# Kernel tuning notes

Hardware: AMD Instinct MI355X
Metric: run time of the kernel (lower is better)

## Reference

```python
import jax, jax.numpy as jnp
import numpy as np

L, D, H, DH, FF, V, B, T, WD, BAND = 4, 512, 8, 64, 2048, 32000, 2, 1024, 32, 128
SCALE = 1.0 / float(np.sqrt(DH))

# per-head causal masks: even heads full causal, odd heads banded causal (0 <= i-j < BAND)
_diff = np.arange(T)[:, None] - np.arange(T)[None, :]
_full = _diff >= 0
_band = _full & (_diff < BAND)
MASKS = jnp.asarray(np.where((np.arange(H) % 2 == 0)[:, None, None], _full, _band))  # (H,T,T) bool
# ALiBi slopes for H=8 (power of 2): start=ratio=2^(-2^(-(log2(8)-3)))=0.5 -> 0.5^(1..8)
_slopes = 0.5 ** np.arange(1, H + 1)
ALIBI = jnp.asarray((-_slopes[:, None, None] * _diff).astype(np.float32))  # (H,T,T)


def _ln(x, g, b):
    m = x.mean(-1, keepdims=True)
    v = ((x - m) ** 2).mean(-1, keepdims=True)
    return (x - m) / jnp.sqrt(v + 1e-5) * g + b


def setup_inputs() -> dict:
    key = jax.random.key(0)
    ks = jax.random.split(key, 16)
    s = 0.02
    n = lambda k, shape: jax.random.normal(k, shape, jnp.float32) * s
    return dict(
        idx=jax.random.randint(ks[0], (B, T), 0, V),
        wte=n(ks[1], (V, D)), wpe=n(ks[2], (T, D)),
        ln1_g=jnp.ones((L, D)), ln1_b=jnp.zeros((L, D)),
        attn_w=n(ks[3], (L, 3 * D, D)), attn_b=jnp.zeros((L, 3 * D)),
        proj_w=n(ks[4], (L, D, D)), proj_b=jnp.zeros((L, D)),
        dape_gw=n(ks[5], (L, WD, 2 * H)), dape_gb=jnp.zeros((L, WD)),
        dape_vw=n(ks[6], (L, WD, 2 * H)), dape_vb=jnp.zeros((L, WD)),
        dape_ow=n(ks[7], (L, H, WD)), dape_ob=jnp.zeros((L, H)),
        ln2_g=jnp.ones((L, D)), ln2_b=jnp.zeros((L, D)),
        gate_w=n(ks[8], (L, FF, D)), gate_b=jnp.zeros((L, FF)),
        val_w=n(ks[9], (L, FF, D)), val_b=jnp.zeros((L, FF)),
        mlp_w=n(ks[10], (L, D, FF)), mlp_b=jnp.zeros((L, D)),
        lnf_g=jnp.ones((D,)), lnf_b=jnp.zeros((D,)),
        lm_w=n(ks[11], (V, D)),
    )


def reference(idx, wte, wpe, ln1_g, ln1_b, attn_w, attn_b, proj_w, proj_b,
              dape_gw, dape_gb, dape_vw, dape_vb, dape_ow, dape_ob,
              ln2_g, ln2_b, gate_w, gate_b, val_w, val_b, mlp_w, mlp_b,
              lnf_g, lnf_b, lm_w):
    x = wte[idx] + wpe[jnp.arange(T)][None]  # (B,T,D)
    for l in range(L):
        h = _ln(x, ln1_g[l], ln1_b[l])
        qkv = h @ attn_w[l].T + attn_b[l]
        q, k, v = jnp.split(qkv, 3, axis=-1)
        q = q.reshape(B, T, H, DH).transpose(0, 2, 1, 3)
        k = k.reshape(B, T, H, DH).transpose(0, 2, 1, 3)
        v = v.reshape(B, T, H, DH).transpose(0, 2, 1, 3)
        att = jnp.einsum('bhqd,bhkd->bhqk', q, k) * SCALE  # (B,H,T,T)
        # DAPE: concat(att, zero base bias) along head dim, pointwise SWIGLU MLP 2H->WD->H
        cat = jnp.concatenate([att, jnp.zeros_like(att)], axis=1).transpose(0, 2, 3, 1)  # (B,T,T,2H)
        hid = jax.nn.silu(cat @ dape_gw[l].T + dape_gb[l]) * (cat @ dape_vw[l].T + dape_vb[l])
        lb = hid @ dape_ow[l].T + dape_ob[l]  # (B,T,T,H)
        att = att + lb.transpose(0, 3, 1, 2) + ALIBI[None]
        att = jnp.where(MASKS[None], att, -jnp.inf)
        att = jax.nn.softmax(att, axis=-1)
        y = jnp.einsum('bhqk,bhkd->bhqd', att, v).transpose(0, 2, 1, 3).reshape(B, T, D)
        x = x + y @ proj_w[l].T + proj_b[l]
        h2 = _ln(x, ln2_g[l], ln2_b[l])
        ff = jax.nn.silu(h2 @ gate_w[l].T + gate_b[l]) * (h2 @ val_w[l].T + val_b[l])
        x = x + ff @ mlp_w[l].T + mlp_b[l]
    x = _ln(x, lnf_g, lnf_b)
    return x @ lm_w.T  # (B,T,V)
```

## Files before the change

kernel.cpp:

```cpp
#include <hip/hip_runtime.h>
#include <hip/hip_bf16.h>
#include <math.h>

constexpr int L = 4, D = 512, H = 8, DH = 64, FF = 2048, V = 32000, B = 2, T = 1024, WD = 32, BAND = 128;
constexpr float SCALE = 0.125f;

typedef __hip_bfloat16 bf16;
typedef __attribute__((ext_vector_type(8))) short short8;
typedef __attribute__((ext_vector_type(4))) float floatx4;

#define MFMA16(a, b, c) __builtin_amdgcn_mfma_f32_16x16x32_bf16(a, b, c, 0, 0, 0)

__device__ inline void gl_lds16(const void* g, void* l) {
    __builtin_amdgcn_global_load_lds((const __attribute__((address_space(1))) unsigned int*)g,
                                     (__attribute__((address_space(3))) unsigned int*)l, 16, 0, 0);
}

__global__ __launch_bounds__(256) void embed_k(const int* __restrict__ idx,
                                               const float* __restrict__ wte,
                                               const float* __restrict__ wpe,
                                               float* __restrict__ x) {
    int row = blockIdx.x;
    int t = row % T;
    int token = idx[row];
    const float* we = wte + (size_t)token * D;
    const float* pe = wpe + (size_t)t * D;
    float* xo = x + (size_t)row * D;
    for (int d = threadIdx.x; d < D; d += 256) xo[d] = we[d] + pe[d];
}

__global__ __launch_bounds__(256) void f2b_k(const float* __restrict__ in,
                                             bf16* __restrict__ out, int n4) {
    int i = blockIdx.x * 256 + threadIdx.x;
    if (i >= n4) return;
    float4 v = *(const float4*)&in[(size_t)i * 4];
    bf16 o[4] = {__float2bfloat16(v.x), __float2bfloat16(v.y),
                 __float2bfloat16(v.z), __float2bfloat16(v.w)};
    *(ulong1*)&out[(size_t)i * 4] = *(ulong1*)o;
}

__global__ __launch_bounds__(256) void ln_bf16_k(const float* __restrict__ x,
                                                 const float* __restrict__ g,
                                                 const float* __restrict__ b,
                                                 bf16* __restrict__ o) {
    int row = blockIdx.x;
    const float* xr = x + (size_t)row * D;
    int d0 = threadIdx.x, d1 = threadIdx.x + 256;
    float v0 = xr[d0], v1 = xr[d1];
    float s = v0 + v1, ss = v0 * v0 + v1 * v1;
    for (int off = 32; off > 0; off >>= 1) {
        s  += __shfl_down(s, off);
        ss += __shfl_down(ss, off);
    }
    __shared__ float red[2][4];
    int wid = threadIdx.x >> 6;
    if ((threadIdx.x & 63) == 0) { red[0][wid] = s; red[1][wid] = ss; }
    __syncthreads();
    s  = red[0][0] + red[0][1] + red[0][2] + red[0][3];
    ss = red[1][0] + red[1][1] + red[1][2] + red[1][3];
    float mean = s * (1.0f / D);
    float var  = ss * (1.0f / D) - mean * mean;
    float rstd = rsqrtf(var + 1e-5f);
    bf16* orow = o + (size_t)row * D;
    orow[d0] = __float2bfloat16((v0 - mean) * rstd * g[d0] + b[d0]);
    orow[d1] = __float2bfloat16((v1 - mean) * rstd * g[d1] + b[d1]);
}

template <int EPI>
__global__ __launch_bounds__(256) void mgemm_k(const bf16* __restrict__ A,
                                               const bf16* __restrict__ W,
                                               const float* __restrict__ bias,
                                               const float* res,
                                               float* C, int M, int N, int K) {
    __shared__ __align__(16) bf16 As[128 * 32];
    __shared__ __align__(16) bf16 Bs[128 * 32];
    int tid = threadIdx.x;
    int wave = tid >> 6, lane = tid & 63;
    int quad = lane >> 4, l16 = lane & 15;
    int m0 = blockIdx.y * 128, n0 = blockIdx.x * 128;
    int wm = wave >> 1, wn = wave & 1;
    floatx4 acc[4][4] = {};

    int idx0 = tid, idx1 = tid + 256;
    const bf16* Ag0 = A + (size_t)(m0 + (idx0 >> 2)) * K + (idx0 & 3) * 8;
    const bf16* Ag1 = A + (size_t)(m0 + (idx1 >> 2)) * K + (idx1 & 3) * 8;
    const bf16* Wg0 = W + (size_t)(n0 + (idx0 >> 2)) * K + (idx0 & 3) * 8;
    const bf16* Wg1 = W + (size_t)(n0 + (idx1 >> 2)) * K + (idx1 & 3) * 8;
    bf16* lA0 = As + (size_t)(wave * 64) * 8;
    bf16* lA1 = As + (size_t)(256 + wave * 64) * 8;
    bf16* lB0 = Bs + (size_t)(wave * 64) * 8;
    bf16* lB1 = Bs + (size_t)(256 + wave * 64) * 8;

    for (int k0 = 0; k0 < K; k0 += 32) {
        __syncthreads();
        gl_lds16(Ag0 + k0, lA0);
        gl_lds16(Ag1 + k0, lA1);
        gl_lds16(Wg0 + k0, lB0);
        gl_lds16(Wg1 + k0, lB1);
        __syncthreads();
        short8 a[4], b[4];
#pragma unroll
        for (int mi = 0; mi < 4; mi++)
            a[mi] = *(const short8*)&As[(wm * 64 + mi * 16 + l16) * 32 + quad * 8];
#pragma unroll
        for (int ni = 0; ni < 4; ni++)
            b[ni] = *(const short8*)&Bs[(wn * 64 + ni * 16 + l16) * 32 + quad * 8];
#pragma unroll
        for (int mi = 0; mi < 4; mi++)
#pragma unroll
            for (int ni = 0; ni < 4; ni++)
                acc[mi][ni] = MFMA16(a[mi], b[ni], acc[mi][ni]);
    }

    int row_base = m0 + wm * 64 + quad * 4;
    int col_base = n0 + wn * 64 + l16;
#pragma unroll
    for (int mi = 0; mi < 4; mi++) {
#pragma unroll
        for (int r = 0; r < 4; r++) {
            int m = row_base + mi * 16 + r;
#pragma unroll
            for (int ni = 0; ni < 4; ni++) {
                int n = col_base + ni * 16;
                float v = acc[mi][ni][r];
                if (EPI == 0 || EPI == 1 || EPI == 3) v += bias[n];
                if (EPI == 1) v += res[(size_t)m * N + n];
                if (EPI == 3) {
                    ((bf16*)C)[(size_t)m * N + n] = __float2bfloat16(v);
                } else {
                    C[(size_t)m * N + n] = v;
                }
            }
        }
    }
}

__global__ __launch_bounds__(256) void swiglu_k(const float* __restrict__ g,
                                                const float* __restrict__ v,
                                                bf16* __restrict__ out, int n4) {
    int i = blockIdx.x * 256 + threadIdx.x;
    if (i >= n4) return;
    float4 gv = *(const float4*)&g[(size_t)i * 4];
    float4 vv = *(const float4*)&v[(size_t)i * 4];
    float r0 = gv.x / (1.0f + __expf(-gv.x)) * vv.x;
    float r1 = gv.y / (1.0f + __expf(-gv.y)) * vv.y;
    float r2 = gv.z / (1.0f + __expf(-gv.z)) * vv.z;
    float r3 = gv.w / (1.0f + __expf(-gv.w)) * vv.w;
    bf16 o[4] = {__float2bfloat16(r0), __float2bfloat16(r1),
                 __float2bfloat16(r2), __float2bfloat16(r3)};
    *(ulong1*)&out[(size_t)i * 4] = *(ulong1*)o;
}

__global__ __launch_bounds__(256) void vt_k(const bf16* __restrict__ qkvb,
                                            bf16* __restrict__ vT) {
    int bh = blockIdx.y, b = bh >> 3, h = bh & 7;
    int t0 = blockIdx.x * 64;
    __shared__ bf16 Ls[64][72];
    int tid = threadIdx.x;
#pragma unroll
    for (int it = 0; it < 2; it++) {
        int c = it * 256 + tid;
        int r = c >> 3, s = c & 7;
        *(short8*)&Ls[r][s * 8] =
            *(const short8*)&qkvb[((size_t)(b * T + t0 + r)) * (3 * D) + 2 * D + h * DH + s * 8];
    }
    __syncthreads();
    int d = tid & 63;
    int tg = tid >> 6;
    for (int k = tg; k < 8; k += 4) {
        union { unsigned short u[8]; short8 v; } tmp;
#pragma unroll
        for (int e = 0; e < 8; e++) tmp.u[e] = *(const unsigned short*)&Ls[k * 8 + e][d];
        *(short8*)&vT[((size_t)bh * DH + d) * T + t0 + k * 8] = tmp.v;
    }
}

__global__ __launch_bounds__(256) void qk_mfma_k(const bf16* __restrict__ qkvb,
                                                 float* __restrict__ att) {
    int bh = blockIdx.z; int b = bh >> 3, h = bh & 7;
    int i0 = blockIdx.y * 64, j0 = blockIdx.x * 64;
    if (j0 > i0 + 63) return;
    __shared__ __align__(16) bf16 Qs[64 * 64];
    __shared__ __align__(16) bf16 Ks[64 * 64];
    int tid = threadIdx.x;
    int wave = tid >> 6, lane = tid & 63;
    int l16 = lane & 15, quad = lane >> 4;
    int wi = wave >> 1, wj = wave & 1;

    const bf16* Qbase = qkvb + ((size_t)(b * T + i0)) * (3 * D) + h * DH;
    const bf16* Kbase = qkvb + ((size_t)(b * T + j0)) * (3 * D) + D + h * DH;
#pragma unroll
    for (int it = 0; it < 2; it++) {
        int cbase = it * 256 + wave * 64;
        int c = cbase + lane;
        int r = c >> 3, s = c & 7, gs = s ^ (r & 7);
        gl_lds16(Qbase + (size_t)r * (3 * D) + gs * 8, Qs + (size_t)cbase * 8);
        gl_lds16(Kbase + (size_t)r * (3 * D) + gs * 8, Ks + (size_t)cbase * 8);
    }
    __syncthreads();

    floatx4 acc[2][2] = {};
#pragma unroll
    for (int ks = 0; ks < 2; ks++) {
        short8 a[2], bb[2];
#pragma unroll
        for (int mi = 0; mi < 2; mi++) {
            int row = wi * 32 + mi * 16 + l16;
            a[mi] = *(const short8*)&Qs[row * 64 + (((ks * 4 + quad) ^ (row & 7)) * 8)];
        }
#pragma unroll
        for (int ni = 0; ni < 2; ni++) {
            int row = wj * 32 + ni * 16 + l16;
            bb[ni] = *(const short8*)&Ks[row * 64 + (((ks * 4 + quad) ^ (row & 7)) * 8)];
        }
#pragma unroll
        for (int mi = 0; mi < 2; mi++)
#pragma unroll
            for (int ni = 0; ni < 2; ni++)
                acc[mi][ni] = MFMA16(a[mi], bb[ni], acc[mi][ni]);
    }

    size_t obase = ((size_t)bh * T + (i0 + wi * 32)) * T + (j0 + wj * 32);
#pragma unroll
    for (int mi = 0; mi < 2; mi++)
#pragma unroll
        for (int r = 0; r < 4; r++)
#pragma unroll
            for (int ni = 0; ni < 2; ni++)
                att[obase + (size_t)(mi * 16 + quad * 4 + r) * T + ni * 16 + l16] =
                    acc[mi][ni][r] * SCALE;
}

__global__ __launch_bounds__(256) void dape_sm_k(const float* __restrict__ att,
                                                 bf16* __restrict__ P,
                                                 const float* __restrict__ gw,
                                                 const float* __restrict__ gb,
                                                 const float* __restrict__ vw,
                                                 const float* __restrict__ vb,
                                                 const float* __restrict__ ow,
                                                 const float* __restrict__ ob) {
    int bi = blockIdx.x;
    int b = bi >> 10;
    int i = (T - 1) - (bi & (T - 1));
    int tid = threadIdx.x;
    int wave = tid >> 6, lane = tid & 63;

    __shared__ float4 sgw[WD][2], svw[WD][2], sow[WD][2];
    __shared__ float sgb[WD], svb[WD], sob[H];
    __shared__ float redm[4][8], reds[4][8];
    if (tid < WD) {
        sgw[tid][0] = *(const float4*)&gw[tid * 2 * H];
        sgw[tid][1] = *(const float4*)&gw[tid * 2 * H + 4];
        svw[tid][0] = *(const float4*)&vw[tid * 2 * H];
        svw[tid][1] = *(const float4*)&vw[tid * 2 * H + 4];
        sgb[tid] = gb[tid]; svb[tid] = vb[tid];
        float o0[4], o1[4];
#pragma unroll
        for (int hh = 0; hh < 4; hh++) o0[hh] = ow[hh * WD + tid];
#pragma unroll
        for (int hh = 0; hh < 4; hh++) o1[hh] = ow[(hh + 4) * WD + tid];
        sow[tid][0] = *(float4*)o0;
        sow[tid][1] = *(float4*)o1;
    }
    if (tid < H) sob[tid] = ob[tid];
    __syncthreads();

    const float slopes[8] = {0.5f, 0.25f, 0.125f, 0.0625f,
                             0.03125f, 0.015625f, 0.0078125f, 0.00390625f};
    size_t abase = (size_t)b * H * T * T + (size_t)i * T;

    float sv[4][8];
    int jv[4];
#pragma unroll
    for (int c = 0; c < 4; c++) {
        int j = tid + c * 256;
        jv[c] = j;
        if (j <= i) {
#pragma unroll
            for (int hh = 0; hh < 8; hh++)
                sv[c][hh] = att[abase + (size_t)hh * T * T + j];
        }
    }

    float lb[4][8];
#pragma unroll
    for (int c = 0; c < 4; c++)
#pragma unroll
        for (int hh = 0; hh < 8; hh++) lb[c][hh] = sob[hh];
    for (int w = 0; w < WD; w++) {
        float4 g0 = sgw[w][0], g1 = sgw[w][1];
        float4 v0 = svw[w][0], v1 = svw[w][1];
        float4 o0 = sow[w][0], o1 = sow[w][1];
        float gbb = sgb[w], vbb = svb[w];
#pragma unroll
        for (int c = 0; c < 4; c++) {
            if (jv[c] <= i) {
                float g = gbb + sv[c][0] * g0.x + sv[c][1] * g0.y + sv[c][2] * g0.z + sv[c][3] * g0.w
                              + sv[c][4] * g1.x + sv[c][5] * g1.y + sv[c][6] * g1.z + sv[c][7] * g1.w;
                float v = vbb + sv[c][0] * v0.x + sv[c][1] * v0.y + sv[c][2] * v0.z + sv[c][3] * v0.w
                              + sv[c][4] * v1.x + sv[c][5] * v1.y + sv[c][6] * v1.z + sv[c][7] * v1.w;
                float hid = g / (1.0f + __expf(-g)) * v;
                lb[c][0] += hid * o0.x; lb[c][1] += hid * o0.y;
                lb[c][2] += hid * o0.z; lb[c][3] += hid * o0.w;
                lb[c][4] += hid * o1.x; lb[c][5] += hid * o1.y;
                lb[c][6] += hid * o1.z; lb[c][7] += hid * o1.w;
            }
        }
    }

    float mx[8];
#pragma unroll
    for (int hh = 0; hh < 8; hh++) mx[hh] = -1e30f;
#pragma unroll
    for (int c = 0; c < 4; c++) {
        if (jv[c] <= i) {
            float diff = (float)(i - jv[c]);
#pragma unroll
            for (int hh = 0; hh < 8; hh++) {
                float val = sv[c][hh] + lb[c][hh] - slopes[hh] * diff;
                if ((hh & 1) && (jv[c] < i - (BAND - 1))) val = -1e30f;
                sv[c][hh] = val;
                mx[hh] = fmaxf(mx[hh], val);
            }
        }
    }
    for (int off = 32; off > 0; off >>= 1)
#pragma unroll
        for (int hh = 0; hh < 8; hh++) mx[hh] = fmaxf(mx[hh], __shfl_down(mx[hh], off));
    if (lane == 0)
#pragma unroll
        for (int hh = 0; hh < 8; hh++) redm[wave][hh] = mx[hh];
    __syncthreads();
#pragma unroll
    for (int hh = 0; hh < 8; hh++)
        mx[hh] = fmaxf(fmaxf(redm[0][hh], redm[1][hh]), fmaxf(redm[2][hh], redm[3][hh]));

    float sm[8];
#pragma unroll
    for (int hh = 0; hh < 8; hh++) sm[hh] = 0.f;
#pragma unroll
    for (int c = 0; c < 4; c++) {
        if (jv[c] <= i) {
#pragma unroll
            for (int hh = 0; hh < 8; hh++) {
                float p = __expf(sv[c][hh] - mx[hh]);
                sv[c][hh] = p;
                sm[hh] += p;
            }
        }
    }
    for (int off = 32; off > 0; off >>= 1)
#pragma unroll
        for (int hh = 0; hh < 8; hh++) sm[hh] += __shfl_down(sm[hh], off);
    if (lane == 0)
#pragma unroll
        for (int hh = 0; hh < 8; hh++) reds[wave][hh] = sm[hh];
    __syncthreads();
    float inv[8];
#pragma unroll
    for (int hh = 0; hh < 8; hh++)
        inv[hh] = 1.0f / (reds[0][hh] + reds[1][hh] + reds[2][hh] + reds[3][hh]);

    size_t pbase = (size_t)b * H * T * T + (size_t)i * T;
#pragma unroll
    for (int c = 0; c < 4; c++) {
        if (jv[c] <= i) {
#pragma unroll
            for (int hh = 0; hh < 8; hh++)
                P[pbase + (size_t)hh * T * T + jv[c]] = __float2bfloat16(sv[c][hh] * inv[hh]);
        }
    }
    int ia = i & ~63;
    int zhi = ia + 63;
    for (int j = i + 1 + tid; j <= zhi; j += 256)
#pragma unroll
        for (int hh = 0; hh < 8; hh++)
            P[pbase + (size_t)hh * T * T + j] = __float2bfloat16(0.f);
    int js = (ia - (BAND - 1) > 0 ? ia - (BAND - 1) : 0) & ~31;
    for (int j = js + tid; j <= i - BAND; j += 256)
#pragma unroll
        for (int hh = 1; hh < 8; hh += 2)
            P[pbase + (size_t)hh * T * T + j] = __float2bfloat16(0.f);
}

__global__ __launch_bounds__(256) void av_mfma_k(const bf16* __restrict__ P,
                                                 const bf16* __restrict__ vT,
                                                 bf16* __restrict__ y) {
    int bh = blockIdx.y; int b = bh >> 3, h = bh & 7;
    int ia = blockIdx.x * 64;
    __shared__ __align__(16) bf16 Ps[64 * 32];
    __shared__ __align__(16) bf16 Vs[64 * 32];
    int tid = threadIdx.x, wave = tid >> 6, lane = tid & 63;
    int l16 = lane & 15, quad = lane >> 4;
    int wi = wave >> 1, wn = wave & 1;
    floatx4 acc[2][2] = {};

    int j_end = ia + 63;
    int j_start = (h & 1) ? ((ia - (BAND - 1) > 0 ? ia - (BAND - 1) : 0) & ~31) : 0;
    const bf16* Pbase = P + ((size_t)bh * T + ia) * T;
    const bf16* Vbase = vT + (size_t)bh * DH * T;
    int r = tid >> 2, s = tid & 3, gs = s ^ ((r >> 1) & 3);
    bf16* lP = Ps + (size_t)(wave * 64) * 8;
    bf16* lV = Vs + (size_t)(wave * 64) * 8;

    for (int j0 = j_start; j0 <= j_end; j0 += 32) {
        __syncthreads();
        gl_lds16(Pbase + (size_t)r * T + j0 + gs * 8, lP);
        gl_lds16(Vbase + (size_t)r * T + j0 + gs * 8, lV);
        __syncthreads();
        short8 a[2], bb[2];
#pragma unroll
        for (int mi = 0; mi < 2; mi++) {
            int row = wi * 32 + mi * 16 + l16;
            a[mi] = *(const short8*)&Ps[row * 32 + ((quad ^ ((row >> 1) & 3)) * 8)];
        }
#pragma unroll
        for (int ni = 0; ni < 2; ni++) {
            int row = wn * 32 + ni * 16 + l16;
            bb[ni] = *(const short8*)&Vs[row * 32 + ((quad ^ ((row >> 1) & 3)) * 8)];
        }
#pragma unroll
        for (int mi = 0; mi < 2; mi++)
#pragma unroll
            for (int ni = 0; ni < 2; ni++)
                acc[mi][ni] = MFMA16(a[mi], bb[ni], acc[mi][ni]);
    }

#pragma unroll
    for (int mi = 0; mi < 2; mi++)
#pragma unroll
        for (int rr = 0; rr < 4; rr++) {
            int i = ia + wi * 32 + mi * 16 + quad * 4 + rr;
#pragma unroll
            for (int ni = 0; ni < 2; ni++) {
                int d = wn * 32 + ni * 16 + l16;
                y[((size_t)(b * T + i)) * D + h * DH + d] = __float2bfloat16(acc[mi][ni][rr]);
            }
        }
}

extern "C" void kernel_launch(void* const* d_in, const int* in_sizes, int n_in,
                              void* d_out, int out_size, void* d_ws, size_t ws_size,
                              hipStream_t stream) {
    const int*   idx     = (const int*)d_in[0];
    const float* wte     = (const float*)d_in[1];
    const float* wpe     = (const float*)d_in[2];
    const float* ln1_g   = (const float*)d_in[3];
    const float* ln1_b   = (const float*)d_in[4];
    const float* attn_w  = (const float*)d_in[5];
    const float* attn_b  = (const float*)d_in[6];
    const float* proj_w  = (const float*)d_in[7];
    const float* proj_b  = (const float*)d_in[8];
    const float* dape_gw = (const float*)d_in[9];
    const float* dape_gb = (const float*)d_in[10];
    const float* dape_vw = (const float*)d_in[11];
    const float* dape_vb = (const float*)d_in[12];
    const float* dape_ow = (const float*)d_in[13];
    const float* dape_ob = (const float*)d_in[14];
    const float* ln2_g   = (const float*)d_in[15];
    const float* ln2_b   = (const float*)d_in[16];
    const float* gate_w  = (const float*)d_in[17];
    const float* gate_b  = (const float*)d_in[18];
    const float* val_w   = (const float*)d_in[19];
    const float* val_b   = (const float*)d_in[20];
    const float* mlp_w   = (const float*)d_in[21];
    const float* mlp_b   = (const float*)d_in[22];
    const float* lnf_g   = (const float*)d_in[23];
    const float* lnf_b   = (const float*)d_in[24];
    const float* lm_w    = (const float*)d_in[25];
    float* out = (float*)d_out;

    float* ws   = (float*)d_ws;
    float* x    = ws;
    float* att  = x + (size_t)B * T * D;
    float* gbuf = att;
    float* vbuf = att + (size_t)B * T * FF;
    bf16*  hb   = (bf16*)(att + (size_t)B * H * T * T);
    bf16*  yb   = hb   + (size_t)B * T * D;
    bf16*  ffb  = yb   + (size_t)B * T * D;
    bf16*  qkvb = ffb  + (size_t)B * T * FF;
    bf16*  vTb  = qkvb + (size_t)B * T * 3 * D;
    bf16*  Pb   = vTb  + (size_t)B * H * DH * T;
    bf16*  wq   = Pb   + (size_t)B * H * T * T;
    bf16*  wp   = wq   + (size_t)L * 3 * D * D;
    bf16*  wg   = wp   + (size_t)L * D * D;
    bf16*  wv   = wg   + (size_t)L * FF * D;
    bf16*  wm   = wv   + (size_t)L * FF * D;
    bf16*  wl   = wm   + (size_t)L * D * FF;

    auto conv = [&](const float* src, bf16* dst, size_t n) {
        int n4 = (int)(n / 4);
        f2b_k<<<(n4 + 255) / 256, 256, 0, stream>>>(src, dst, n4);
    };
    conv(attn_w, wq, (size_t)L * 3 * D * D);
    conv(proj_w, wp, (size_t)L * D * D);
    conv(gate_w, wg, (size_t)L * FF * D);
    conv(val_w,  wv, (size_t)L * FF * D);
    conv(mlp_w,  wm, (size_t)L * D * FF);
    conv(lm_w,   wl, (size_t)V * D);

    embed_k<<<B * T, 256, 0, stream>>>(idx, wte, wpe, x);

    const int M = B * T;
    for (int l = 0; l < L; l++) {
        ln_bf16_k<<<M, 256, 0, stream>>>(x, ln1_g + l * D, ln1_b + l * D, hb);
        mgemm_k<3><<<dim3(3 * D / 128, M / 128), 256, 0, stream>>>(
            hb, wq + (size_t)l * 3 * D * D, attn_b + l * 3 * D, nullptr, (float*)qkvb, M, 3 * D, D);
        vt_k<<<dim3(T / 64, B * H), 256, 0, stream>>>(qkvb, vTb);
        qk_mfma_k<<<dim3(T / 64, T / 64, B * H), 256, 0, stream>>>(qkvb, att);
        dape_sm_k<<<B * T, 256, 0, stream>>>(att, Pb,
            dape_gw + l * WD * 2 * H, dape_gb + l * WD,
            dape_vw + l * WD * 2 * H, dape_vb + l * WD,
            dape_ow + l * H * WD, dape_ob + l * H);
        av_mfma_k<<<dim3(T / 64, B * H), 256, 0, stream>>>(Pb, vTb, yb);
        mgemm_k<1><<<dim3(D / 128, M / 128), 256, 0, stream>>>(
            yb, wp + (size_t)l * D * D, proj_b + l * D, x, x, M, D, D);
        ln_bf16_k<<<M, 256, 0, stream>>>(x, ln2_g + l * D, ln2_b + l * D, hb);
        mgemm_k<0><<<dim3(FF / 128, M / 128), 256, 0, stream>>>(
            hb, wg + (size_t)l * FF * D, gate_b + l * FF, nullptr, gbuf, M, FF, D);
        mgemm_k<0><<<dim3(FF / 128, M / 128), 256, 0, stream>>>(
            hb, wv + (size_t)l * FF * D, val_b + l * FF, nullptr, vbuf, M, FF, D);
        {
            int n4 = B * T * FF / 4;
            swiglu_k<<<(n4 + 255) / 256, 256, 0, stream>>>(gbuf, vbuf, ffb, n4);
        }
        mgemm_k<1><<<dim3(D / 128, M / 128), 256, 0, stream>>>(
            ffb, wm + (size_t)l * D * FF, mlp_b + l * D, x, x, M, D, FF);
    }

    ln_bf16_k<<<M, 256, 0, stream>>>(x, lnf_g, lnf_b, hb);
    mgemm_k<2><<<dim3(V / 128, M / 128), 256, 0, stream>>>(
        hb, wl, nullptr, nullptr, out, M, V, D);
}
```

Measured before the change: 1.531 ms.

## Fuse gate/value GEMMs with SwiGLU epilogue and shrink GEMM tiles for small-N

Adds a dual-weight GEMM kernel that computes the gate and value projections together from one shared A tile and applies SiLU-gating in the epilogue, writing bf16 directly. This removes two fp32 intermediate buffers, their round-trip through memory, and the separate swiglu launch. The GEMM kernel is also templated on tile size, and the QKV, proj and MLP-down GEMMs now use 128x64 tiles so more blocks are launched across the CUs. Smaller tiles lower per-block data reuse.

```diff
diff --git a/kernel.cpp b/kernel.cpp
--- a/kernel.cpp
+++ b/kernel.cpp
@@ -66,61 +66,71 @@
     orow[d1] = __float2bfloat16((v1 - mean) * rstd * g[d1] + b[d1]);
 }
 
-template <int EPI>
+template <int BM, int BN, int EPI>
 __global__ __launch_bounds__(256) void mgemm_k(const bf16* __restrict__ A,
                                                const bf16* __restrict__ W,
                                                const float* __restrict__ bias,
                                                const float* res,
                                                float* C, int M, int N, int K) {
-    __shared__ __align__(16) bf16 As[128 * 32];
-    __shared__ __align__(16) bf16 Bs[128 * 32];
+    constexpr int WM = BM / 2, WN = BN / 2;
+    constexpr int FM = WM / 16, FN = WN / 16;
+    constexpr int CA = BM / 64, CB = BN / 64;
+    __shared__ __align__(16) bf16 As[BM * 32];
+    __shared__ __align__(16) bf16 Bs[BN * 32];
     int tid = threadIdx.x;
     int wave = tid >> 6, lane = tid & 63;
     int quad = lane >> 4, l16 = lane & 15;
-    int m0 = blockIdx.y * 128, n0 = blockIdx.x * 128;
+    int m0 = blockIdx.y * BM, n0 = blockIdx.x * BN;
     int wm = wave >> 1, wn = wave & 1;
-    floatx4 acc[4][4] = {};
-
-    int idx0 = tid, idx1 = tid + 256;
-    const bf16* Ag0 = A + (size_t)(m0 + (idx0 >> 2)) * K + (idx0 & 3) * 8;
-    const bf16* Ag1 = A + (size_t)(m0 + (idx1 >> 2)) * K + (idx1 & 3) * 8;
-    const bf16* Wg0 = W + (size_t)(n0 + (idx0 >> 2)) * K + (idx0 & 3) * 8;
-    const bf16* Wg1 = W + (size_t)(n0 + (idx1 >> 2)) * K + (idx1 & 3) * 8;
-    bf16* lA0 = As + (size_t)(wave * 64) * 8;
-    bf16* lA1 = As + (size_t)(256 + wave * 64) * 8;
-    bf16* lB0 = Bs + (size_t)(wave * 64) * 8;
-    bf16* lB1 = Bs + (size_t)(256 + wave * 64) * 8;
+    floatx4 acc[FM][FN] = {};
+
+    const bf16* Ag[CA];
+    const bf16* Wg[CB];
+    bf16* lA[CA];
+    bf16* lB[CB];
+#pragma unroll
+    for (int c = 0; c < CA; c++) {
+        int idx = c * 256 + tid;
+        Ag[c] = A + (size_t)(m0 + (idx >> 2)) * K + (idx & 3) * 8;
+        lA[c] = As + (size_t)(c * 256 + wave * 64) * 8;
+    }
+#pragma unroll
+    for (int c = 0; c < CB; c++) {
+        int idx = c * 256 + tid;
+        Wg[c] = W + (size_t)(n0 + (idx >> 2)) * K + (idx & 3) * 8;
+        lB[c] = Bs + (size_t)(c * 256 + wave * 64) * 8;
+    }
 
     for (int k0 = 0; k0 < K; k0 += 32) {
         __syncthreads();
-        gl_lds16(Ag0 + k0, lA0);
-        gl_lds16(Ag1 + k0, lA1);
-        gl_lds16(Wg0 + k0, lB0);
-        gl_lds16(Wg1 + k0, lB1);
+#pragma unroll
+        for (int c = 0; c < CA; c++) gl_lds16(Ag[c] + k0, lA[c]);
+#pragma unroll
+        for (int c = 0; c < CB; c++) gl_lds16(Wg[c] + k0, lB[c]);
         __syncthreads();
-        short8 a[4], b[4];
-#pragma unroll
-        for (int mi = 0; mi < 4; mi++)
-            a[mi] = *(const short8*)&As[(wm * 64 + mi * 16 + l16) * 32 + quad * 8];
-#pragma unroll
-        for (int ni = 0; ni < 4; ni++)
-            b[ni] = *(const short8*)&Bs[(wn * 64 + ni * 16 + l16) * 32 + quad * 8];
-#pragma unroll
-        for (int mi = 0; mi < 4; mi++)
-#pragma unroll
-            for (int ni = 0; ni < 4; ni++)
+        short8 a[FM], b[FN];
+#pragma unroll
+        for (int mi = 0; mi < FM; mi++)
+            a[mi] = *(const short8*)&As[(wm * WM + mi * 16 + l16) * 32 + quad * 8];
+#pragma unroll
+        for (int ni = 0; ni < FN; ni++)
+            b[ni] = *(const short8*)&Bs[(wn * WN + ni * 16 + l16) * 32 + quad * 8];
+#pragma unroll
+        for (int mi = 0; mi < FM; mi++)
+#pragma unroll
+            for (int ni = 0; ni < FN; ni++)
                 acc[mi][ni] = MFMA16(a[mi], b[ni], acc[mi][ni]);
     }
 
-    int row_base = m0 + wm * 64 + quad * 4;
-    int col_base = n0 + wn * 64 + l16;
-#pragma unroll
-    for (int mi = 0; mi < 4; mi++) {
+    int row_base = m0 + wm * WM + quad * 4;
+    int col_base = n0 + wn * WN + l16;
+#pragma unroll
+    for (int mi = 0; mi < FM; mi++) {
 #pragma unroll
         for (int r = 0; r < 4; r++) {
             int m = row_base + mi * 16 + r;
 #pragma unroll
-            for (int ni = 0; ni < 4; ni++) {
+            for (int ni = 0; ni < FN; ni++) {
                 int n = col_base + ni * 16;
                 float v = acc[mi][ni][r];
                 if (EPI == 0 || EPI == 1 || EPI == 3) v += bias[n];
@@ -135,20 +145,76 @@
     }
 }
 
-__global__ __launch_bounds__(256) void swiglu_k(const float* __restrict__ g,
-                                                const float* __restrict__ v,
-                                                bf16* __restrict__ out, int n4) {
-    int i = blockIdx.x * 256 + threadIdx.x;
-    if (i >= n4) return;
-    float4 gv = *(const float4*)&g[(size_t)i * 4];
-    float4 vv = *(const float4*)&v[(size_t)i * 4];
-    float r0 = gv.x / (1.0f + __expf(-gv.x)) * vv.x;
-    float r1 = gv.y / (1.0f + __expf(-gv.y)) * vv.y;
-    float r2 = gv.z / (1.0f + __expf(-gv.z)) * vv.z;
-    float r3 = gv.w / (1.0f + __expf(-gv.w)) * vv.w;
-    bf16 o[4] = {__float2bfloat16(r0), __float2bfloat16(r1),
-                 __float2bfloat16(r2), __float2bfloat16(r3)};
-    *(ulong1*)&out[(size_t)i * 4] = *(ulong1*)o;
+__global__ __launch_bounds__(256) void mgemm_glu_k(const bf16* __restrict__ A,
+                                                   const bf16* __restrict__ Wgp,
+                                                   const bf16* __restrict__ Wvp,
+                                                   const float* __restrict__ gbias,
+                                                   const float* __restrict__ vbias,
+                                                   bf16* __restrict__ O,
+                                                   int M, int N, int K) {
+    constexpr int BM = 128, BN = 64, WM = 64, WN = 32, FM = 4, FN = 2;
+    __shared__ __align__(16) bf16 As[BM * 32];
+    __shared__ __align__(16) bf16 Gs[BN * 32];
+    __shared__ __align__(16) bf16 Vs[BN * 32];
+    int tid = threadIdx.x;
+    int wave = tid >> 6, lane = tid & 63;
+    int quad = lane >> 4, l16 = lane & 15;
+    int m0 = blockIdx.y * BM, n0 = blockIdx.x * BN;
+    int wm = wave >> 1, wn = wave & 1;
+    floatx4 accg[FM][FN] = {}, accv[FM][FN] = {};
+
+    int idx0 = tid, idx1 = tid + 256;
+    const bf16* Ag0 = A + (size_t)(m0 + (idx0 >> 2)) * K + (idx0 & 3) * 8;
+    const bf16* Ag1 = A + (size_t)(m0 + (idx1 >> 2)) * K + (idx1 & 3) * 8;
+    const bf16* Gg = Wgp + (size_t)(n0 + (idx0 >> 2)) * K + (idx0 & 3) * 8;
+    const bf16* Vg = Wvp + (size_t)(n0 + (idx0 >> 2)) * K + (idx0 & 3) * 8;
+    bf16* lA0 = As + (size_t)(wave * 64) * 8;
+    bf16* lA1 = As + (size_t)(256 + wave * 64) * 8;
+    bf16* lG = Gs + (size_t)(wave * 64) * 8;
+    bf16* lV = Vs + (size_t)(wave * 64) * 8;
+
+    for (int k0 = 0; k0 < K; k0 += 32) {
+        __syncthreads();
+        gl_lds16(Ag0 + k0, lA0);
+        gl_lds16(Ag1 + k0, lA1);
+        gl_lds16(Gg + k0, lG);
+        gl_lds16(Vg + k0, lV);
+        __syncthreads();
+        short8 a[FM], g[FN], v[FN];
+#pragma unroll
+        for (int mi = 0; mi < FM; mi++)
+            a[mi] = *(const short8*)&As[(wm * WM + mi * 16 + l16) * 32 + quad * 8];
+#pragma unroll
+        for (int ni = 0; ni < FN; ni++) {
+            g[ni] = *(const short8*)&Gs[(wn * WN + ni * 16 + l16) * 32 + quad * 8];
+            v[ni] = *(const short8*)&Vs[(wn * WN + ni * 16 + l16) * 32 + quad * 8];
+        }
+#pragma unroll
+        for (int mi = 0; mi < FM; mi++)
+#pragma unroll
+            for (int ni = 0; ni < FN; ni++) {
+                accg[mi][ni] = MFMA16(a[mi], g[ni], accg[mi][ni]);
+                accv[mi][ni] = MFMA16(a[mi], v[ni], accv[mi][ni]);
+            }
+    }
+
+    int row_base = m0 + wm * WM + quad * 4;
+    int col_base = n0 + wn * WN + l16;
+#pragma unroll
+    for (int mi = 0; mi < FM; mi++) {
+#pragma unroll
+        for (int r = 0; r < 4; r++) {
+            int m = row_base + mi * 16 + r;
+#pragma unroll
+            for (int ni = 0; ni < FN; ni++) {
+                int n = col_base + ni * 16;
+                float gv = accg[mi][ni][r] + gbias[n];
+                float vv = accv[mi][ni][r] + vbias[n];
+                float o = gv / (1.0f + __expf(-gv)) * vv;
+                O[(size_t)m * N + n] = __float2bfloat16(o);
+            }
+        }
+    }
 }
 
 __global__ __launch_bounds__(256) void vt_k(const bf16* __restrict__ qkvb,
@@ -473,8 +539,6 @@
     float* ws   = (float*)d_ws;
     float* x    = ws;
     float* att  = x + (size_t)B * T * D;
-    float* gbuf = att;
-    float* vbuf = att + (size_t)B * T * FF;
     bf16*  hb   = (bf16*)(att + (size_t)B * H * T * T);
     bf16*  yb   = hb   + (size_t)B * T * D;
     bf16*  ffb  = yb   + (size_t)B * T * D;
@@ -504,7 +568,7 @@
     const int M = B * T;
     for (int l = 0; l < L; l++) {
         ln_bf16_k<<<M, 256, 0, stream>>>(x, ln1_g + l * D, ln1_b + l * D, hb);
-        mgemm_k<3><<<dim3(3 * D / 128, M / 128), 256, 0, stream>>>(
+        mgemm_k<128, 64, 3><<<dim3(3 * D / 64, M / 128), 256, 0, stream>>>(
             hb, wq + (size_t)l * 3 * D * D, attn_b + l * 3 * D, nullptr, (float*)qkvb, M, 3 * D, D);
         vt_k<<<dim3(T / 64, B * H), 256, 0, stream>>>(qkvb, vTb);
         qk_mfma_k<<<dim3(T / 64, T / 64, B * H), 256, 0, stream>>>(qkvb, att);
@@ -513,22 +577,17 @@
             dape_vw + l * WD * 2 * H, dape_vb + l * WD,
             dape_ow + l * H * WD, dape_ob + l * H);
         av_mfma_k<<<dim3(T / 64, B * H), 256, 0, stream>>>(Pb, vTb, yb);
-        mgemm_k<1><<<dim3(D / 128, M / 128), 256, 0, stream>>>(
+        mgemm_k<128, 64, 1><<<dim3(D / 64, M / 128), 256, 0, stream>>>(
             yb, wp + (size_t)l * D * D, proj_b + l * D, x, x, M, D, D);
         ln_bf16_k<<<M, 256, 0, stream>>>(x, ln2_g + l * D, ln2_b + l * D, hb);
-        mgemm_k<0><<<dim3(FF / 128, M / 128), 256, 0, stream>>>(
-            hb, wg + (size_t)l * FF * D, gate_b + l * FF, nullptr, gbuf, M, FF, D);
-        mgemm_k<0><<<dim3(FF / 128, M / 128), 256, 0, stream>>>(
-            hb, wv + (size_t)l * FF * D, val_b + l * FF, nullptr, vbuf, M, FF, D);
-        {
-            int n4 = B * T * FF / 4;
-            swiglu_k<<<(n4 + 255) / 256, 256, 0, stream>>>(gbuf, vbuf, ffb, n4);
-        }
-        mgemm_k<1><<<dim3(D / 128, M / 128), 256, 0, stream>>>(
+        mgemm_glu_k<<<dim3(FF / 64, M / 128), 256, 0, stream>>>(
+            hb, wg + (size_t)l * FF * D, wv + (size_t)l * FF * D,
+            gate_b + l * FF, val_b + l * FF, ffb, M, FF, D);
+        mgemm_k<128, 64, 1><<<dim3(D / 64, M / 128), 256, 0, stream>>>(
             ffb, wm + (size_t)l * D * FF, mlp_b + l * D, x, x, M, D, FF);
     }
 
     ln_bf16_k<<<M, 256, 0, stream>>>(x, lnf_g, lnf_b, hb);
-    mgemm_k<2><<<dim3(V / 128, M / 128), 256, 0, stream>>>(
+    mgemm_k<128, 128, 2><<<dim3(V / 128, M / 128), 256, 0, stream>>>(
         hb, wl, nullptr, nullptr, out, M, V, D);
 }
```

After: 1.327 ms. 1.15x faster.
